# Kernel tuning notes

Hardware: AMD Instinct MI355X
Metric: run time of the kernel (lower is better)

Reference implementation:

```python
import jax, jax.numpy as jnp
import numpy as np

N_HEAD = 16

def setup_inputs() -> dict:
    key = jax.random.key(0)
    ks = jax.random.split(key, 9)
    C = 1024
    s = 1.0 / np.sqrt(C)
    x = jax.random.normal(ks[0], (2, 2048, C), dtype=jnp.float32)
    Wq = jax.random.normal(ks[1], (C, C), dtype=jnp.float32) * s
    Wk = jax.random.normal(ks[2], (C, C), dtype=jnp.float32) * s
    Wv = jax.random.normal(ks[3], (C, C), dtype=jnp.float32) * s
    Wp = jax.random.normal(ks[4], (C, C), dtype=jnp.float32) * s
    z = jnp.zeros((C,), dtype=jnp.float32)
    return {"x": x, "Wq": Wq, "bq": z, "Wk": Wk, "bk": z, "Wv": Wv, "bv": z, "Wp": Wp, "bp": z}

def reference(x, Wq, bq, Wk, bk, Wv, bv, Wp, bp):
    B, T, C = x.shape
    H = N_HEAD
    D = C // H
    # QKV projections (Linear: x @ W.T + b), split heads -> [B, H, T, D]
    q = (x @ Wq.T + bq).reshape(B, T, H, D).transpose(0, 2, 1, 3)
    k = (x @ Wk.T + bk).reshape(B, T, H, D).transpose(0, 2, 1, 3)
    v = (x @ Wv.T + bv).reshape(B, T, H, D).transpose(0, 2, 1, 3)
    scale = 1.0 / jnp.sqrt(jnp.asarray(D, dtype=x.dtype))  # scaled_attn=True
    att = jnp.einsum('bhtd,bhsd->bhts', q, k) * scale      # [B,H,T,T]
    att = jax.nn.softmax(att, axis=-1)
    y = jnp.einsum('bhts,bhsd->bhtd', att, v)              # [B,H,T,D]
    y = y.transpose(0, 2, 1, 3).reshape(B, T, C)
    return y @ Wp.T + bp
```

## Files before the change

kernel.cpp:

```cpp
#include <hip/hip_runtime.h>
#include <stdint.h>

typedef unsigned short u16;
typedef __attribute__((ext_vector_type(8))) short short8;
typedef __attribute__((ext_vector_type(4))) float float4v;
typedef __attribute__((ext_vector_type(4))) u16 ushort4v;
typedef __attribute__((ext_vector_type(2))) unsigned int uint2v;

#define MFMA_BF16(a, b, c) __builtin_amdgcn_mfma_f32_16x16x32_bf16((a), (b), (c), 0, 0, 0)

__device__ __forceinline__ u16 f2bf(float f) {
    uint32_t u = __builtin_bit_cast(uint32_t, f);
    u += 0x7FFFu + ((u >> 16) & 1u);
    return (u16)(u >> 16);
}
__device__ __forceinline__ void g2l16(const void* g, void* l) {
    __builtin_amdgcn_global_load_lds(
        (const __attribute__((address_space(1))) void*)g,
        (__attribute__((address_space(3))) void*)l, 16, 0, 0);
}

__global__ void cast_all(const float* __restrict__ x, const float* __restrict__ wq,
                         const float* __restrict__ wk, const float* __restrict__ wv,
                         const float* __restrict__ wp,
                         u16* __restrict__ xb, u16* __restrict__ wqkvb, u16* __restrict__ wpb) {
    int bx = blockIdx.x;
    const float* src; u16* dst; int base;
    if (bx < 4096)      { src = x;  dst = xb;              base = bx; }
    else if (bx < 5120) { src = wq; dst = wqkvb;           base = bx - 4096; }
    else if (bx < 6144) { src = wk; dst = wqkvb + 1048576; base = bx - 5120; }
    else if (bx < 7168) { src = wv; dst = wqkvb + 2097152; base = bx - 6144; }
    else                { src = wp; dst = wpb;             base = bx - 7168; }
    int i = base * 1024 + threadIdx.x * 4;
    float4v v = *(const float4v*)(src + i);
    ushort4v o;
    #pragma unroll
    for (int r = 0; r < 4; ++r) o[r] = f2bf(v[r]);
    *(ushort4v*)(dst + i) = o;
}

__device__ __forceinline__ void gemm_core_128(const u16* __restrict__ A, const u16* __restrict__ B,
                                              int K, int m0, int n0, float4v acc[4][4]) {
    __shared__ u16 lA[128 * 64];
    __shared__ u16 lB[128 * 64];
    const int tid = threadIdx.x, lane = tid & 63;
    const int wave = tid >> 6, wm = wave >> 1, wn = wave & 1;
    const int l15 = lane & 15, quad = lane >> 4;
    const int sw7 = l15 & 7;

    for (int kt = 0; kt < K; kt += 64) {
        __syncthreads();
        #pragma unroll
        for (int i = 0; i < 4; ++i) {
            int f = i * 256 + tid;
            int row = f >> 3, kc = f & 7;
            int gcol = (kc ^ (row & 7)) * 8;
            g2l16(A + (size_t)(m0 + row) * K + kt + gcol, &lA[f * 8]);
            g2l16(B + (size_t)(n0 + row) * K + kt + gcol, &lB[f * 8]);
        }
        __syncthreads();
        #pragma unroll
        for (int ks = 0; ks < 2; ++ks) {
            short8 af[4], bf[4];
            #pragma unroll
            for (int t = 0; t < 4; ++t) {
                int pc = ((ks * 4 + quad) ^ sw7) * 8;
                af[t] = *(const short8*)&lA[(wm * 64 + t * 16 + l15) * 64 + pc];
                bf[t] = *(const short8*)&lB[(wn * 64 + t * 16 + l15) * 64 + pc];
            }
            #pragma unroll
            for (int tm = 0; tm < 4; ++tm)
                #pragma unroll
                for (int tn = 0; tn < 4; ++tn)
                    acc[tm][tn] = MFMA_BF16(af[tm], bf[tn], acc[tm][tn]);
        }
    }
}

__global__ __launch_bounds__(256, 2) void gemm_qkv(
    const u16* __restrict__ xb, const u16* __restrict__ wqkv,
    const float* __restrict__ bq, const float* __restrict__ bk, const float* __restrict__ bv,
    u16* __restrict__ qo, u16* __restrict__ ko, u16* __restrict__ vto) {
    const int bx = blockIdx.x, by = blockIdx.y;
    const int tid = threadIdx.x, lane = tid & 63;
    const int wave = tid >> 6, wm = wave >> 1, wn = wave & 1;
    const int l15 = lane & 15, quad = lane >> 4;
    const float QSC = 0.125f * 1.44269504088896340736f;

    if (bx < 16) {
        float4v acc[4][4] = {};
        gemm_core_128(wqkv, xb, 1024, bx * 128, by * 128, acc);
        const bool isq = bx < 8;
        const float* bvec = isq ? bq : bk;
        u16* dst = isq ? qo : ko;
        #pragma unroll
        for (int tm = 0; tm < 4; ++tm) {
            int nloc = (bx & 7) * 128 + wm * 64 + tm * 16 + quad * 4;
            int h = nloc >> 6, d0 = nloc & 63;
            float4v bias = *(const float4v*)(bvec + nloc);
            #pragma unroll
            for (int tn = 0; tn < 4; ++tn) {
                int t = by * 128 + wn * 64 + tn * 16 + l15;
                int b = t >> 11, tt = t & 2047;
                ushort4v pk;
                #pragma unroll
                for (int r = 0; r < 4; ++r) {
                    float v = acc[tm][tn][r] + bias[r];
                    pk[r] = f2bf(isq ? v * QSC : v);
                }
                *(ushort4v*)&dst[(((size_t)(b * 16 + h)) * 2048 + tt) * 64 + d0] = pk;
            }
        }
    } else {
        float4v acc[4][4] = {};
        gemm_core_128(xb, wqkv, 1024, by * 128, bx * 128, acc);
        #pragma unroll
        for (int tn = 0; tn < 4; ++tn) {
            int n = bx * 128 + wn * 64 + tn * 16 + l15;
            int cb = n & 1023, h = cb >> 6, d = cb & 63;
            float bias = bv[cb];
            #pragma unroll
            for (int tm = 0; tm < 4; ++tm) {
                int mb = by * 128 + wm * 64 + tm * 16 + quad * 4;
                int b = mb >> 11, t0 = mb & 2047;
                ushort4v pk;
                #pragma unroll
                for (int r = 0; r < 4; ++r) pk[r] = f2bf(acc[tm][tn][r] + bias);
                *(ushort4v*)&vto[(((size_t)(b * 16 + h)) * 64 + d) * 2048 + t0] = pk;
            }
        }
    }
}

__global__ __launch_bounds__(256, 2) void gemm_out(
    const u16* __restrict__ yb, const u16* __restrict__ wpb,
    const float* __restrict__ bp, float* __restrict__ out) {
    float4v acc[4][4] = {};
    gemm_core_128(wpb, yb, 1024, blockIdx.x * 128, blockIdx.y * 128, acc);
    const int tid = threadIdx.x, lane = tid & 63;
    const int wave = tid >> 6, wm = wave >> 1, wn = wave & 1;
    const int l15 = lane & 15, quad = lane >> 4;
    #pragma unroll
    for (int tm = 0; tm < 4; ++tm) {
        int n = blockIdx.x * 128 + wm * 64 + tm * 16 + quad * 4;
        float4v bias = *(const float4v*)(bp + n);
        #pragma unroll
        for (int tn = 0; tn < 4; ++tn) {
            int t = blockIdx.y * 128 + wn * 64 + tn * 16 + l15;
            float4v o;
            #pragma unroll
            for (int r = 0; r < 4; ++r) o[r] = acc[tm][tn][r] + bias[r];
            *(float4v*)&out[(size_t)t * 1024 + n] = o;
        }
    }
}

__global__ __launch_bounds__(256, 2) void attn(
    const u16* __restrict__ qg, const u16* __restrict__ kg,
    const u16* __restrict__ vtg, u16* __restrict__ yb) {
    __shared__ __attribute__((aligned(16))) char smem[54272];
    u16* kb0 = (u16*)smem;
    u16* pb  = (u16*)(smem + 32768);
    float* lsum = (float*)(smem + 53248);
    float* red  = (float*)smem;

    const int tid = threadIdx.x, lane = tid & 63;
    const int w = tid >> 6;
    const int l15 = lane & 15, quad = lane >> 4, sw7 = l15 & 7;
    const int bh = blockIdx.y, qt0 = blockIdx.x * 64;

    const u16* qbase = qg + (size_t)bh * 2048 * 64;
    const u16* kbase = kg + (size_t)bh * 2048 * 64;
    const u16* vtbase = vtg + (size_t)bh * 64 * 2048;
    u16* pw = pb + w * 2560;

    short8 qf[4][2];
    #pragma unroll
    for (int tn = 0; tn < 4; ++tn)
        #pragma unroll
        for (int ks = 0; ks < 2; ++ks)
            qf[tn][ks] = *(const short8*)(qbase + (size_t)(qt0 + tn * 16 + l15) * 64 + ks * 32 + quad * 8);

    float4v oacc[4][4] = {};
    float rs[4] = {};

    {
        #pragma unroll
        for (int i = 0; i < 4; ++i) {
            int f = i * 256 + tid, row = f >> 3, kc = f & 7;
            g2l16(kbase + (size_t)row * 64 + (kc ^ (row & 7)) * 8, &kb0[f * 8]);
        }
    }

    for (int it = 0; it < 16; ++it) {
        __syncthreads();
        if (it + 1 < 16) {
            u16* nb = kb0 + ((it + 1) & 1) * 8192;
            const u16* src = kbase + (size_t)(it + 1) * 128 * 64;
            #pragma unroll
            for (int i = 0; i < 4; ++i) {
                int f = i * 256 + tid, row = f >> 3, kc = f & 7;
                g2l16(src + (size_t)row * 64 + (kc ^ (row & 7)) * 8, &nb[f * 8]);
            }
        }
        const u16* kbu = kb0 + (it & 1) * 8192;
        float4v sacc[2][4] = {};
        #pragma unroll
        for (int ks = 0; ks < 2; ++ks) {
            short8 kf[2];
            #pragma unroll
            for (int tm = 0; tm < 2; ++tm)
                kf[tm] = *(const short8*)&kbu[(w * 32 + tm * 16 + l15) * 64 + (((ks * 4 + quad) ^ sw7)) * 8];
            #pragma unroll
            for (int tm = 0; tm < 2; ++tm)
                #pragma unroll
                for (int tn = 0; tn < 4; ++tn)
                    sacc[tm][tn] = MFMA_BF16(kf[tm], qf[tn][ks], sacc[tm][tn]);
        }
        #pragma unroll
        for (int tm = 0; tm < 2; ++tm)
            #pragma unroll
            for (int tn = 0; tn < 4; ++tn) {
                uint32_t u[4];
                #pragma unroll
                for (int r = 0; r < 4; ++r) {
                    float p = __builtin_amdgcn_exp2f(sacc[tm][tn][r]);
                    u[r] = __builtin_bit_cast(uint32_t, p);
                    rs[tn] += __builtin_bit_cast(float, u[r] & 0xFFFF0000u);
                }
                uint2v pk;
                pk.x = __builtin_amdgcn_perm(u[1], u[0], 0x07060302u);
                pk.y = __builtin_amdgcn_perm(u[3], u[2], 0x07060302u);
                *(uint2v*)&pw[(tn * 16 + l15) * 40 + tm * 16 + quad * 4] = pk;
            }
        short8 vf[4];
        #pragma unroll
        for (int tmm = 0; tmm < 4; ++tmm)
            vf[tmm] = *(const short8*)(vtbase + (size_t)(tmm * 16 + l15) * 2048 + it * 128 + w * 32 + quad * 8);
        short8 bfn[4];
        #pragma unroll
        for (int tnn = 0; tnn < 4; ++tnn)
            bfn[tnn] = *(const short8*)&pw[(tnn * 16 + l15) * 40 + quad * 8];
        #pragma unroll
        for (int tmm = 0; tmm < 4; ++tmm)
            #pragma unroll
            for (int tnn = 0; tnn < 4; ++tnn)
                oacc[tmm][tnn] = MFMA_BF16(vf[tmm], bfn[tnn], oacc[tmm][tnn]);
    }
    #pragma unroll
    for (int tn = 0; tn < 4; ++tn) {
        float v = rs[tn];
        v += __shfl_xor(v, 16);
        v += __shfl_xor(v, 32);
        rs[tn] = v;
    }
    if (lane < 16)
        #pragma unroll
        for (int tn = 0; tn < 4; ++tn)
            lsum[w * 64 + tn * 16 + l15] = rs[tn];
    __syncthreads();
    if (w > 0) {
        float* dst = red + (w - 1) * 4096;
        #pragma unroll
        for (int tmm = 0; tmm < 4; ++tmm)
            #pragma unroll
            for (int tnn = 0; tnn < 4; ++tnn)
                *(float4v*)&dst[((tmm * 4 + tnn) * 64 + lane) * 4] = oacc[tmm][tnn];
    }
    __syncthreads();
    if (w == 0) {
        const int b = bh >> 4, h = bh & 15;
        #pragma unroll
        for (int tmm = 0; tmm < 4; ++tmm)
            #pragma unroll
            for (int tnn = 0; tnn < 4; ++tnn) {
                float4v s = oacc[tmm][tnn];
                #pragma unroll
                for (int ww = 0; ww < 3; ++ww) {
                    float4v o = *(const float4v*)&red[(ww * 4096) + ((tmm * 4 + tnn) * 64 + lane) * 4];
                    #pragma unroll
                    for (int r = 0; r < 4; ++r) s[r] += o[r];
                }
                oacc[tmm][tnn] = s;
            }
        #pragma unroll
        for (int tnn = 0; tnn < 4; ++tnn) {
            int q = tnn * 16 + l15;
            float inv = 1.0f / (lsum[q] + lsum[64 + q] + lsum[128 + q] + lsum[192 + q]);
            #pragma unroll
            for (int tmm = 0; tmm < 4; ++tmm) {
                int d0 = tmm * 16 + quad * 4;
                ushort4v pk;
                #pragma unroll
                for (int r = 0; r < 4; ++r) pk[r] = f2bf(oacc[tmm][tnn][r] * inv);
                *(ushort4v*)&yb[((size_t)(b * 2048 + qt0 + q)) * 1024 + h * 64 + d0] = pk;
            }
        }
    }
}

extern "C" void kernel_launch(void* const* d_in, const int* in_sizes, int n_in,
                              void* d_out, int out_size, void* d_ws, size_t ws_size,
                              hipStream_t stream) {
    const float* x  = (const float*)d_in[0];
    const float* Wq = (const float*)d_in[1];
    const float* bq = (const float*)d_in[2];
    const float* Wk = (const float*)d_in[3];
    const float* bk = (const float*)d_in[4];
    const float* Wv = (const float*)d_in[5];
    const float* bv = (const float*)d_in[6];
    const float* Wp = (const float*)d_in[7];
    const float* bp = (const float*)d_in[8];
    float* out = (float*)d_out;
    uint8_t* ws = (uint8_t*)d_ws;

    u16* xb   = (u16*)(ws);
    u16* wqkv = (u16*)(ws + (8u << 20));
    u16* wpb  = (u16*)(ws + (14u << 20));
    u16* qb   = (u16*)(ws + (16u << 20));
    u16* kb   = (u16*)(ws + (24u << 20));
    u16* vtb  = (u16*)(ws + (32u << 20));
    u16* yb   = (u16*)(ws + (40u << 20));

    cast_all<<<8192, 256, 0, stream>>>(x, Wq, Wk, Wv, Wp, xb, wqkv, wpb);
    gemm_qkv<<<dim3(24, 32), 256, 0, stream>>>(xb, wqkv, bq, bk, bv, qb, kb, vtb);
    attn<<<dim3(32, 32), 256, 0, stream>>>(qb, kb, vtb, yb);
    gemm_out<<<dim3(8, 32), 256, 0, stream>>>(yb, wpb, bp, out);
}
```

Before: 196.5 us.

## Stage QK epilogue through LDS, swap out-GEMM operands, compute row sums via MFMA

The Q/K projection epilogue now writes results into shared memory and then stores them to global memory as 16-byte rows. This replaces the scattered 8-byte stores. The output GEMM swaps its A and B operands, so its epilogue writes scalar floats with lanes spread along n. Attention drops the per-element softmax denominator accumulation and cross-lane shuffles, computing row sums with an extra MFMA against a ones vector. It also hoists the V loads ahead of the QK^T computation to hide their latency. The trade-offs are an extra MFMA per tile, more LDS round-trips and barriers in the QKV epilogue, and scalar stores in the output GEMM that may coalesce less well.

```diff
diff --git a/kernel.cpp b/kernel.cpp
--- a/kernel.cpp
+++ b/kernel.cpp
@@ -5,6 +5,7 @@
 typedef __attribute__((ext_vector_type(8))) short short8;
 typedef __attribute__((ext_vector_type(4))) float float4v;
 typedef __attribute__((ext_vector_type(4))) u16 ushort4v;
+typedef __attribute__((ext_vector_type(4))) unsigned int uint4v;
 typedef __attribute__((ext_vector_type(2))) unsigned int uint2v;
 
 #define MFMA_BF16(a, b, c) __builtin_amdgcn_mfma_f32_16x16x32_bf16((a), (b), (c), 0, 0, 0)
@@ -40,9 +41,8 @@
 }
 
 __device__ __forceinline__ void gemm_core_128(const u16* __restrict__ A, const u16* __restrict__ B,
-                                              int K, int m0, int n0, float4v acc[4][4]) {
-    __shared__ u16 lA[128 * 64];
-    __shared__ u16 lB[128 * 64];
+                                              int K, int m0, int n0,
+                                              u16* lA, u16* lB, float4v acc[4][4]) {
     const int tid = threadIdx.x, lane = tid & 63;
     const int wave = tid >> 6, wm = wave >> 1, wn = wave & 1;
     const int l15 = lane & 15, quad = lane >> 4;
@@ -81,6 +81,7 @@
     const u16* __restrict__ xb, const u16* __restrict__ wqkv,
     const float* __restrict__ bq, const float* __restrict__ bk, const float* __restrict__ bv,
     u16* __restrict__ qo, u16* __restrict__ ko, u16* __restrict__ vto) {
+    __shared__ __attribute__((aligned(16))) u16 ls[16384];
     const int bx = blockIdx.x, by = blockIdx.y;
     const int tid = threadIdx.x, lane = tid & 63;
     const int wave = tid >> 6, wm = wave >> 1, wn = wave & 1;
@@ -89,31 +90,47 @@
 
     if (bx < 16) {
         float4v acc[4][4] = {};
-        gemm_core_128(wqkv, xb, 1024, bx * 128, by * 128, acc);
+        gemm_core_128(wqkv, xb, 1024, bx * 128, by * 128, ls, ls + 8192, acc);
         const bool isq = bx < 8;
         const float* bvec = isq ? bq : bk;
         u16* dst = isq ? qo : ko;
-        #pragma unroll
-        for (int tm = 0; tm < 4; ++tm) {
-            int nloc = (bx & 7) * 128 + wm * 64 + tm * 16 + quad * 4;
-            int h = nloc >> 6, d0 = nloc & 63;
-            float4v bias = *(const float4v*)(bvec + nloc);
-            #pragma unroll
-            for (int tn = 0; tn < 4; ++tn) {
-                int t = by * 128 + wn * 64 + tn * 16 + l15;
-                int b = t >> 11, tt = t & 2047;
-                ushort4v pk;
-                #pragma unroll
-                for (int r = 0; r < 4; ++r) {
-                    float v = acc[tm][tn][r] + bias[r];
-                    pk[r] = f2bf(isq ? v * QSC : v);
+        const int b = by >> 4;
+        #pragma unroll
+        for (int h = 0; h < 2; ++h) {
+            __syncthreads();
+            if (wm == h) {
+                #pragma unroll
+                for (int tm = 0; tm < 4; ++tm) {
+                    int fl = tm * 16 + quad * 4;
+                    int nloc = (bx & 7) * 128 + h * 64 + fl;
+                    float4v bias = *(const float4v*)(bvec + nloc);
+                    #pragma unroll
+                    for (int tn = 0; tn < 4; ++tn) {
+                        int t = wn * 64 + tn * 16 + l15;
+                        ushort4v pk;
+                        #pragma unroll
+                        for (int r = 0; r < 4; ++r) {
+                            float v = acc[tm][tn][r] + bias[r];
+                            pk[r] = f2bf(isq ? v * QSC : v);
+                        }
+                        *(ushort4v*)&ls[t * 72 + fl] = pk;
+                    }
                 }
-                *(ushort4v*)&dst[(((size_t)(b * 16 + h)) * 2048 + tt) * 64 + d0] = pk;
+            }
+            __syncthreads();
+            int hg = (bx & 7) * 2 + h;
+            int c8 = (tid & 7) * 8, tr = tid >> 3;
+            #pragma unroll
+            for (int rnd = 0; rnd < 4; ++rnd) {
+                int t = rnd * 32 + tr;
+                uint4v v = *(const uint4v*)&ls[t * 72 + c8];
+                int tg = (by * 128 + t) & 2047;
+                *(uint4v*)&dst[(((size_t)(b * 16 + hg)) * 2048 + tg) * 64 + c8] = v;
             }
         }
     } else {
         float4v acc[4][4] = {};
-        gemm_core_128(xb, wqkv, 1024, by * 128, bx * 128, acc);
+        gemm_core_128(xb, wqkv, 1024, by * 128, bx * 128, ls, ls + 8192, acc);
         #pragma unroll
         for (int tn = 0; tn < 4; ++tn) {
             int n = bx * 128 + wn * 64 + tn * 16 + l15;
@@ -135,22 +152,23 @@
 __global__ __launch_bounds__(256, 2) void gemm_out(
     const u16* __restrict__ yb, const u16* __restrict__ wpb,
     const float* __restrict__ bp, float* __restrict__ out) {
+    __shared__ __attribute__((aligned(16))) u16 ls[16384];
     float4v acc[4][4] = {};
-    gemm_core_128(wpb, yb, 1024, blockIdx.x * 128, blockIdx.y * 128, acc);
+    gemm_core_128(yb, wpb, 1024, blockIdx.y * 128, blockIdx.x * 128, ls, ls + 8192, acc);
     const int tid = threadIdx.x, lane = tid & 63;
     const int wave = tid >> 6, wm = wave >> 1, wn = wave & 1;
     const int l15 = lane & 15, quad = lane >> 4;
     #pragma unroll
-    for (int tm = 0; tm < 4; ++tm) {
-        int n = blockIdx.x * 128 + wm * 64 + tm * 16 + quad * 4;
-        float4v bias = *(const float4v*)(bp + n);
-        #pragma unroll
-        for (int tn = 0; tn < 4; ++tn) {
-            int t = blockIdx.y * 128 + wn * 64 + tn * 16 + l15;
-            float4v o;
-            #pragma unroll
-            for (int r = 0; r < 4; ++r) o[r] = acc[tm][tn][r] + bias[r];
-            *(float4v*)&out[(size_t)t * 1024 + n] = o;
+    for (int tn = 0; tn < 4; ++tn) {
+        int n = blockIdx.x * 128 + wn * 64 + tn * 16 + l15;
+        float bias = bp[n];
+        #pragma unroll
+        for (int tm = 0; tm < 4; ++tm) {
+            #pragma unroll
+            for (int r = 0; r < 4; ++r) {
+                int m = blockIdx.y * 128 + wm * 64 + tm * 16 + quad * 4 + r;
+                out[(size_t)m * 1024 + n] = acc[tm][tn][r] + bias;
+            }
         }
     }
 }
@@ -174,6 +192,10 @@
     const u16* vtbase = vtg + (size_t)bh * 64 * 2048;
     u16* pw = pb + w * 2560;
 
+    short8 ones;
+    #pragma unroll
+    for (int j = 0; j < 8; ++j) ones[j] = (short)0x3F80;
+
     short8 qf[4][2];
     #pragma unroll
     for (int tn = 0; tn < 4; ++tn)
@@ -182,14 +204,12 @@
             qf[tn][ks] = *(const short8*)(qbase + (size_t)(qt0 + tn * 16 + l15) * 64 + ks * 32 + quad * 8);
 
     float4v oacc[4][4] = {};
-    float rs[4] = {};
-
-    {
-        #pragma unroll
-        for (int i = 0; i < 4; ++i) {
-            int f = i * 256 + tid, row = f >> 3, kc = f & 7;
-            g2l16(kbase + (size_t)row * 64 + (kc ^ (row & 7)) * 8, &kb0[f * 8]);
-        }
+    float4v osum[4] = {};
+
+    #pragma unroll
+    for (int i = 0; i < 4; ++i) {
+        int f = i * 256 + tid, row = f >> 3, kc = f & 7;
+        g2l16(kbase + (size_t)row * 64 + (kc ^ (row & 7)) * 8, &kb0[f * 8]);
     }
 
     for (int it = 0; it < 16; ++it) {
@@ -203,6 +223,10 @@
                 g2l16(src + (size_t)row * 64 + (kc ^ (row & 7)) * 8, &nb[f * 8]);
             }
         }
+        short8 vf[4];
+        #pragma unroll
+        for (int tmm = 0; tmm < 4; ++tmm)
+            vf[tmm] = *(const short8*)(vtbase + (size_t)(tmm * 16 + l15) * 2048 + it * 128 + w * 32 + quad * 8);
         const u16* kbu = kb0 + (it & 1) * 8192;
         float4v sacc[2][4] = {};
         #pragma unroll
@@ -223,20 +247,13 @@
             for (int tn = 0; tn < 4; ++tn) {
                 uint32_t u[4];
                 #pragma unroll
-                for (int r = 0; r < 4; ++r) {
-                    float p = __builtin_amdgcn_exp2f(sacc[tm][tn][r]);
-                    u[r] = __builtin_bit_cast(uint32_t, p);
-                    rs[tn] += __builtin_bit_cast(float, u[r] & 0xFFFF0000u);
-                }
+                for (int r = 0; r < 4; ++r)
+                    u[r] = __builtin_bit_cast(uint32_t, __builtin_amdgcn_exp2f(sacc[tm][tn][r]));
                 uint2v pk;
                 pk.x = __builtin_amdgcn_perm(u[1], u[0], 0x07060302u);
                 pk.y = __builtin_amdgcn_perm(u[3], u[2], 0x07060302u);
                 *(uint2v*)&pw[(tn * 16 + l15) * 40 + tm * 16 + quad * 4] = pk;
             }
-        short8 vf[4];
-        #pragma unroll
-        for (int tmm = 0; tmm < 4; ++tmm)
-            vf[tmm] = *(const short8*)(vtbase + (size_t)(tmm * 16 + l15) * 2048 + it * 128 + w * 32 + quad * 8);
         short8 bfn[4];
         #pragma unroll
         for (int tnn = 0; tnn < 4; ++tnn)
@@ -246,18 +263,14 @@
             #pragma unroll
             for (int tnn = 0; tnn < 4; ++tnn)
                 oacc[tmm][tnn] = MFMA_BF16(vf[tmm], bfn[tnn], oacc[tmm][tnn]);
-    }
-    #pragma unroll
-    for (int tn = 0; tn < 4; ++tn) {
-        float v = rs[tn];
-        v += __shfl_xor(v, 16);
-        v += __shfl_xor(v, 32);
-        rs[tn] = v;
+        #pragma unroll
+        for (int tnn = 0; tnn < 4; ++tnn)
+            osum[tnn] = MFMA_BF16(ones, bfn[tnn], osum[tnn]);
     }
     if (lane < 16)
         #pragma unroll
         for (int tn = 0; tn < 4; ++tn)
-            lsum[w * 64 + tn * 16 + l15] = rs[tn];
+            lsum[w * 64 + tn * 16 + l15] = osum[tn][0];
     __syncthreads();
     if (w > 0) {
         float* dst = red + (w - 1) * 4096;
```

Measured after the change: 205.3 us. 1.04x slower.
